# Performance work log

Hardware: AMD Instinct MI355X
Metric: run time of the kernel (lower is better)

## Reference

```python
import jax, jax.numpy as jnp
import numpy as np

NUM_TREES = 100
VOCAB = 100000
DIM = 32            # dim_leaf_emb
ATT = DIM // 2      # att_dim = 16
BS = 1024

# pair indices matching itertools.combinations(range(n), 2)
_ROW, _COL = np.triu_indices(NUM_TREES, k=1)


def setup_inputs() -> dict:
    key = jax.random.key(0)
    ks = jax.random.split(key, 12)
    x = jax.random.randint(ks[0], (BS, NUM_TREES), 0, VOCAB)
    Emb = jax.random.normal(ks[1], (VOCAB, DIM), dtype=jnp.float32) * 0.02
    W = jax.random.normal(ks[2], (DIM, ATT), dtype=jnp.float32) * (1.0 / np.sqrt(DIM))
    b = jnp.zeros((ATT,), dtype=jnp.float32)
    h = jax.random.normal(ks[3], (ATT,), dtype=jnp.float32) * 0.1
    W1 = jax.random.normal(ks[4], (DIM, DIM // 2), dtype=jnp.float32) * (1.0 / np.sqrt(DIM))
    b1 = jnp.zeros((DIM // 2,), dtype=jnp.float32)
    W2 = jax.random.normal(ks[5], (DIM // 2, DIM // 4), dtype=jnp.float32) * (1.0 / np.sqrt(DIM // 2))
    b2 = jnp.zeros((DIM // 4,), dtype=jnp.float32)
    Wf = jax.random.normal(ks[6], (DIM // 4, 1), dtype=jnp.float32) * (1.0 / np.sqrt(DIM // 4))
    bf = jnp.zeros((1,), dtype=jnp.float32)
    return {"x": x, "Emb": Emb, "W": W, "b": b, "h": h,
            "W1": W1, "b1": b1, "W2": W2, "b2": b2, "Wf": Wf, "bf": bf}


def reference(x, Emb, W, b, h, W1, b1, W2, b2, Wf, bf):
    e = Emb[x]                                   # (bs, T, D)
    half_bip = e[:, _ROW] * e[:, _COL]           # (bs, P, D), P = T*(T-1)/2
    s = jax.nn.relu(jnp.einsum('bpd,da->bpa', half_bip, W) + b)  # (bs, P, A)
    att = jax.nn.softmax(jnp.einsum('bpa,a->bp', s, h), axis=-1) # (bs, P)
    pooled = jnp.einsum('bpd,bp->bd', half_bip, att)             # (bs, D)
    o = jax.nn.relu(pooled @ W1 + b1)
    o = jax.nn.relu(o @ W2 + b2)
    return jax.nn.sigmoid(o @ Wf + bf)           # (bs, 1)
```

## Files before the change

kernel.cpp:

```cpp
#include <hip/hip_runtime.h>
#include <math.h>

constexpr int kT = 100;
constexpr int kD = 32;
constexpr int kA = 16;
constexpr int kESH = 40;
constexpr int kRows = 116;
constexpr int kNT = 512;

typedef float    float4v __attribute__((ext_vector_type(4)));
typedef __fp16   fp16x2  __attribute__((ext_vector_type(2)));
typedef __fp16   half4   __attribute__((ext_vector_type(4)));
typedef __fp16   half8   __attribute__((ext_vector_type(8)));
typedef _Float16 half8v  __attribute__((ext_vector_type(8)));

#if __has_builtin(__builtin_amdgcn_exp2f)
#define EXP2F(x) __builtin_amdgcn_exp2f(x)
#else
#define EXP2F(x) exp2f(x)
#endif

__global__ __launch_bounds__(kNT, 8)
void afm_kernel(const int* __restrict__ x,
                const float* __restrict__ Emb,
                const float* __restrict__ W,
                const float* __restrict__ bb,
                const float* __restrict__ h,
                const float* __restrict__ W1,
                const float* __restrict__ b1,
                const float* __restrict__ W2,
                const float* __restrict__ b2,
                const float* __restrict__ Wf,
                const float* __restrict__ bf,
                float* __restrict__ out)
{
    __shared__ __align__(16) unsigned char smem[18432];
    __shared__ float red[8];
    __shared__ float sh_pooled[kD];
    __shared__ float sh_o1[kA];
    __shared__ float sh_o2[8];

    __fp16* she = (__fp16*)smem;
    const char* sheb = (const char*)smem;

    const int tid  = threadIdx.x;
    const int b    = blockIdx.x;
    const int lane = tid & 63;
    const int wv   = tid >> 6;
    const int quad = lane >> 4;
    const int l15  = lane & 15;
    const int k0   = quad * 8;

    const int* xb = x + b * kT;
    for (int i = tid; i < kT * 8; i += kNT) {
        const int row = i >> 3, c4 = i & 7;
        const int v = xb[row];
        const float4 val = ((const float4*)Emb)[v * 8 + c4];
        union { fp16x2 h2[2]; half4 h4; } tmp;
        tmp.h2[0] = __builtin_amdgcn_cvt_pkrtz(val.x, val.y);
        tmp.h2[1] = __builtin_amdgcn_cvt_pkrtz(val.z, val.w);
        *(half4*)(she + row * kESH + c4 * 4) = tmp.h4;
    }
    if (tid < (kRows - kT) * kESH / 2)
        ((unsigned int*)she)[kT * kESH / 2 + tid] = 0u;

    union { fp16x2 h2[4]; half8v h8; } wa;
#pragma unroll
    for (int j = 0; j < 4; ++j)
        wa.h2[j] = __builtin_amdgcn_cvt_pkrtz(W[(k0 + 2 * j) * kA + l15],
                                              W[(k0 + 2 * j + 1) * kA + l15]);
    float h_reg[4];
    float4v bfrag;
#pragma unroll
    for (int rg = 0; rg < 4; ++rg) {
        h_reg[rg] = h[quad * 4 + rg] * 1.44269504088896340736f;
        bfrag[rg] = bb[quad * 4 + rg];
    }
    const int lane_base = l15 * 80 + quad * 16;
    __syncthreads();

    fp16x2 pool2[4];
    const fp16x2 zz = {(__fp16)0.0f, (__fp16)0.0f};
#pragma unroll
    for (int j = 0; j < 4; ++j) pool2[j] = zz;
    float lsum = 0.0f;

    union HB { half8 fp; fp16x2 h2[4]; half8v mf; };

    auto do_tile = [&](const half8& er, int coff, int rem, bool mask) {
        HB hb;
        hb.fp = er * (*(const half8*)(sheb + coff));
        float4v acc = __builtin_amdgcn_mfma_f32_16x16x32_f16(wa.h8, hb.mf, bfrag, 0, 0, 0);
        float part = 0.0f;
#pragma unroll
        for (int rg = 0; rg < 4; ++rg)
            part = fmaf(fmaxf(acc[rg], 0.0f), h_reg[rg], part);
        part += __shfl_xor(part, 16, 64);
        part += __shfl_xor(part, 32, 64);
        float w = EXP2F(part);
        if (mask) w = (l15 < rem) ? w : 0.0f;
        lsum += w;
        const fp16x2 ww = __builtin_amdgcn_cvt_pkrtz(w, w);
#pragma unroll
        for (int j = 0; j < 4; ++j)
            pool2[j] += ww * hb.h2[j];
    };

    auto do_row = [&](int r) {
        const int len = 99 - r;
        const int nfull = (len - 1) >> 4;
        const half8 er = *(const half8*)(sheb + r * 80 + quad * 16);
        int coff = (r + 1) * 80 + lane_base;
        for (int j = 0; j < nfull; ++j, coff += 1280)
            do_tile(er, coff, 16, false);
        do_tile(er, coff, len - (nfull << 4), true);
    };

    for (int g = 0; g < 6; ++g) {
        const int wvg = (wv + g) & 7;
        do_row(g * 16 + wvg);
        do_row(g * 16 + 15 - wvg);
    }
    if (wv < 3) do_row(96 + wv);

#pragma unroll
    for (int off = 1; off < 64; off <<= 1) lsum += __shfl_xor(lsum, off, 64);
    if (lane == 0) red[wv] = lsum;

    __syncthreads();
    float* stg = (float*)smem;
#pragma unroll
    for (int j = 0; j < 4; ++j) {
        stg[tid * 9 + 2 * j]     = (float)pool2[j][0];
        stg[tid * 9 + 2 * j + 1] = (float)pool2[j][1];
    }
    __syncthreads();

    if (tid < kD) {
        const float invS = 4.0f / (red[0] + red[1] + red[2] + red[3] +
                                   red[4] + red[5] + red[6] + red[7]);
        const int q = tid >> 3, j = tid & 7;
        float s = 0.0f;
        for (int w8 = 0; w8 < 8; ++w8)
            for (int l = 0; l < 16; ++l)
                s += stg[(w8 * 64 + q * 16 + l) * 9 + j];
        sh_pooled[tid] = s * invS;
    }
    __syncthreads();

    if (tid < kA) {
        float o = b1[tid];
#pragma unroll
        for (int d = 0; d < kD; ++d) o = fmaf(sh_pooled[d], W1[d * kA + tid], o);
        sh_o1[tid] = fmaxf(o, 0.0f);
    }
    __syncthreads();
    if (tid < 8) {
        float o = b2[tid];
#pragma unroll
        for (int a = 0; a < kA; ++a) o = fmaf(sh_o1[a], W2[a * 8 + tid], o);
        sh_o2[tid] = fmaxf(o, 0.0f);
    }
    __syncthreads();
    if (tid == 0) {
        float z = bf[0];
#pragma unroll
        for (int j = 0; j < 8; ++j) z = fmaf(sh_o2[j], Wf[j], z);
        out[b] = 1.0f / (1.0f + __expf(-z));
    }
}

extern "C" void kernel_launch(void* const* d_in, const int* in_sizes, int n_in,
                              void* d_out, int out_size, void* d_ws, size_t ws_size,
                              hipStream_t stream) {
    const int*   x   = (const int*)d_in[0];
    const float* Emb = (const float*)d_in[1];
    const float* W   = (const float*)d_in[2];
    const float* bb  = (const float*)d_in[3];
    const float* h   = (const float*)d_in[4];
    const float* W1  = (const float*)d_in[5];
    const float* b1  = (const float*)d_in[6];
    const float* W2  = (const float*)d_in[7];
    const float* b2  = (const float*)d_in[8];
    const float* Wf  = (const float*)d_in[9];
    const float* bf  = (const float*)d_in[10];
    float* out = (float*)d_out;

    afm_kernel<<<1024, kNT, 0, stream>>>(x, Emb, W, bb, h, W1, b1, W2, b2, Wf, bf, out);
}
```

Measured before the change: 107.0 us.

## Process row pairs per tile sharing column loads and pack shuffle reductions

Rows are now processed in adjacent pairs (r, r+1) that share each loaded column tile, issuing two MFMAs per column fragment and masking the extra diagonal element for the second row. The two partial scores are packed into one fp16x2 so each cross-quad shuffle reduction serves both rows. A constant table assigns row pairs to waves for load balance. This halves LDS column reads and shuffle count per pair, at the cost of reducing the attention logits in fp16 precision and slightly more wasted lanes.

```diff
diff --git a/kernel.cpp b/kernel.cpp
--- a/kernel.cpp
+++ b/kernel.cpp
@@ -19,6 +19,18 @@
 #else
 #define EXP2F(x) exp2f(x)
 #endif
+
+__device__ __constant__ unsigned char kRP[50] = {
+    0, 2, 10, 18, 42,
+    1, 3, 11, 19, 43,
+    4, 5, 12, 20, 34,
+    6, 7, 13, 21, 35,
+    8, 14, 22, 26, 27, 36,
+    9, 15, 23, 28, 29, 37,
+    16, 17, 24, 30, 31, 38,
+    25, 32, 33, 39, 40, 41, 44, 45, 46, 47, 48, 49
+};
+__device__ __constant__ unsigned char kRPoff[9] = {0, 5, 10, 15, 20, 26, 32, 38, 50};
 
 __global__ __launch_bounds__(kNT, 8)
 void afm_kernel(const int* __restrict__ x,
@@ -87,41 +99,58 @@
 
     union HB { half8 fp; fp16x2 h2[4]; half8v mf; };
 
-    auto do_tile = [&](const half8& er, int coff, int rem, bool mask) {
-        HB hb;
-        hb.fp = er * (*(const half8*)(sheb + coff));
-        float4v acc = __builtin_amdgcn_mfma_f32_16x16x32_f16(wa.h8, hb.mf, bfrag, 0, 0, 0);
-        float part = 0.0f;
-#pragma unroll
-        for (int rg = 0; rg < 4; ++rg)
-            part = fmaf(fmaxf(acc[rg], 0.0f), h_reg[rg], part);
-        part += __shfl_xor(part, 16, 64);
-        part += __shfl_xor(part, 32, 64);
-        float w = EXP2F(part);
-        if (mask) w = (l15 < rem) ? w : 0.0f;
-        lsum += w;
-        const fp16x2 ww = __builtin_amdgcn_cvt_pkrtz(w, w);
-#pragma unroll
-        for (int j = 0; j < 4; ++j)
-            pool2[j] += ww * hb.h2[j];
+    auto do_tile = [&](const half8& er1, const half8& er2, int coff,
+                       bool first, int rem) {
+        HB hb1, hb2;
+        const half8 ec = *(const half8*)(sheb + coff);
+        hb1.fp = er1 * ec;
+        hb2.fp = er2 * ec;
+        float4v s1 = __builtin_amdgcn_mfma_f32_16x16x32_f16(wa.h8, hb1.mf, bfrag, 0, 0, 0);
+        float4v s2 = __builtin_amdgcn_mfma_f32_16x16x32_f16(wa.h8, hb2.mf, bfrag, 0, 0, 0);
+        float p1 = 0.0f, p2 = 0.0f;
+#pragma unroll
+        for (int rg = 0; rg < 4; ++rg) {
+            p1 = fmaf(fmaxf(s1[rg], 0.0f), h_reg[rg], p1);
+            p2 = fmaf(fmaxf(s2[rg], 0.0f), h_reg[rg], p2);
+        }
+        union { fp16x2 hh; int ii; } t0, t1;
+        t0.hh = __builtin_amdgcn_cvt_pkrtz(p1, p2);
+        t1.ii = __shfl_xor(t0.ii, 16, 64);
+        t0.hh = t0.hh + t1.hh;
+        t1.ii = __shfl_xor(t0.ii, 32, 64);
+        t0.hh = t0.hh + t1.hh;
+        float w1 = EXP2F((float)t0.hh[0]);
+        float w2 = EXP2F((float)t0.hh[1]);
+        if (first) w2 = (l15 > 0) ? w2 : 0.0f;
+        if (rem < 16) {
+            const bool v = l15 < rem;
+            w1 = v ? w1 : 0.0f;
+            w2 = v ? w2 : 0.0f;
+        }
+        lsum += w1 + w2;
+        const fp16x2 ww1 = __builtin_amdgcn_cvt_pkrtz(w1, w1);
+        const fp16x2 ww2 = __builtin_amdgcn_cvt_pkrtz(w2, w2);
+#pragma unroll
+        for (int j = 0; j < 4; ++j) pool2[j] += ww1 * hb1.h2[j];
+#pragma unroll
+        for (int j = 0; j < 4; ++j) pool2[j] += ww2 * hb2.h2[j];
     };
 
-    auto do_row = [&](int r) {
-        const int len = 99 - r;
-        const int nfull = (len - 1) >> 4;
-        const half8 er = *(const half8*)(sheb + r * 80 + quad * 16);
-        int coff = (r + 1) * 80 + lane_base;
-        for (int j = 0; j < nfull; ++j, coff += 1280)
-            do_tile(er, coff, 16, false);
-        do_tile(er, coff, len - (nfull << 4), true);
-    };
-
-    for (int g = 0; g < 6; ++g) {
-        const int wvg = (wv + g) & 7;
-        do_row(g * 16 + wvg);
-        do_row(g * 16 + 15 - wvg);
-    }
-    if (wv < 3) do_row(96 + wv);
+    const int beg = kRPoff[wv], fin = kRPoff[wv + 1];
+    for (int ii = beg; ii < fin; ++ii) {
+        const int r1 = 2 * (int)kRP[ii];
+        const int len = 99 - r1;
+        const int ntiles = (len + 15) >> 4;
+        const half8 er1 = *(const half8*)(sheb + r1 * 80 + quad * 16);
+        const half8 er2 = *(const half8*)(sheb + r1 * 80 + 80 + quad * 16);
+        int coff = (r1 + 1) * 80 + lane_base;
+        do_tile(er1, er2, coff, true, ntiles == 1 ? len : 99);
+        coff += 1280;
+        for (int j = 1; j < ntiles - 1; ++j, coff += 1280)
+            do_tile(er1, er2, coff, false, 99);
+        if (ntiles > 1)
+            do_tile(er1, er2, coff, false, len - ((ntiles - 1) << 4));
+    }
 
 #pragma unroll
     for (int off = 1; off < 64; off <<= 1) lsum += __shfl_xor(lsum, off, 64);
```

Measured after the change: 108.5 us. Within noise of the previous version (+1.3%).
